# Optimization experiments

Hardware: AMD Instinct MI355X
Metric: run time of the kernel (lower is better)

Reference implementation:

```python
import jax, jax.numpy as jnp
import numpy as np

N = 3072          # num nodes
H = 256           # hidden_features
B = 4             # num_heads
HD = H // B       # per-head dim
PRIOR_MU = 1.0
PRIOR_SIGMA = 1.0
LN_EPS = 1e-5


def setup_inputs() -> dict:
    key = jax.random.key(0)
    ks = jax.random.split(key, 12)
    s = 0.02  # weight init scale
    return {
        "h": jax.random.normal(ks[0], (N, H), jnp.float32),
        "gamma": jnp.ones((H,), jnp.float32),
        "beta": jnp.zeros((H,), jnp.float32),
        "W_k": jax.random.normal(ks[1], (H, H), jnp.float32) * s,
        "b_k": jnp.zeros((H,), jnp.float32),
        "W_mu": jax.random.normal(ks[2], (H, H), jnp.float32) * s,
        "b_mu": jnp.zeros((H,), jnp.float32),
        "W_ls": jax.random.normal(ks[3], (H, H), jnp.float32) * s,
        "b_ls": jnp.zeros((H,), jnp.float32),
        "W_v": jax.random.normal(ks[4], (H * B, H), jnp.float32) * s,
        "b_v": jnp.zeros((H,), jnp.float32),
        "diffusion": jax.random.uniform(ks[5], (N, N, 1), jnp.float32),
        "eps": jax.random.normal(ks[6], (N, N, B), jnp.float32),
    }


def reference(h, gamma, beta, W_k, b_k, W_mu, b_mu, W_ls, b_ls, W_v, b_v, diffusion, eps):
    h0 = h
    # LayerNorm
    mean = jnp.mean(h, axis=-1, keepdims=True)
    var = jnp.var(h, axis=-1, keepdims=True)
    hn = (h - mean) * jax.lax.rsqrt(var + LN_EPS) * gamma + beta
    # Q/K-style projections, split into heads: [N, HD, B]
    k = (hn @ W_k + b_k).reshape(N, HD, B)
    mu = (hn @ W_mu + b_mu).reshape(N, HD, B)
    ls = (hn @ W_ls + b_ls).reshape(N, HD, B)
    scale = HD ** -0.5
    mu = jnp.einsum('xyb,zyb->xzb', k, mu) * scale       # [N, N, B]
    ls = jnp.einsum('xyb,zyb->xzb', k, ls) * scale       # [N, N, B]
    sigma = jax.nn.softplus(ls)
    # KL(LogNormal(mu, sigma) || LogNormal(log(prior_mu), prior_sigma))
    mu_p = jnp.log(jnp.asarray(PRIOR_MU, h.dtype))
    sig_p = jnp.asarray(PRIOR_SIGMA, h.dtype)
    kl = (jnp.log(sig_p / sigma)
          + (sigma ** 2 + (mu - mu_p) ** 2) / (2.0 * sig_p ** 2)
          - 0.5)
    kl = (kl * jnp.sign(diffusion)).sum(-1).mean()
    # reparameterized LogNormal sample, masked by diffusion matrix
    a = jnp.exp(mu + sigma * eps) * diffusion            # [N, N, B]
    # L1 normalize over source-node axis (dim=-2), torch F.normalize semantics
    denom = jnp.clip(jnp.sum(jnp.abs(a), axis=-2, keepdims=True), 1e-12)
    a = a / denom
    # diffusion-weighted aggregation: [N, B, H] -> [N, B*H]
    out = jnp.einsum('xyb,yz->xbz', a, hn).reshape(N, B * H)
    out = out @ W_v + b_v                                 # fc_v (dropout = eval mode)
    out = jax.nn.elu(out) + h0
    return out, kl
```

## Files before the change

### kernel.cpp

```cpp
#include <hip/hip_runtime.h>
#include <hip/hip_bf16.h>


#define NN 3072
#define HH 256
#define NB 4
#define HD 64
constexpr int KMLSZ = 192 * 2 * 64 * 8;

typedef __attribute__((ext_vector_type(8))) short bf16x8;
typedef __attribute__((ext_vector_type(4))) float f32x4;

static __device__ inline short f2bf(float f) {
    __hip_bfloat16 h = __float2bfloat16(f);
    return __builtin_bit_cast(short, h);
}

__global__ void k0_prep(const float* __restrict__ Wk, const float* __restrict__ Wmu,
                        const float* __restrict__ Wls, const float* __restrict__ bk,
                        const float* __restrict__ bmu, const float* __restrict__ bls,
                        const float* __restrict__ Wv, short* __restrict__ WTcat,
                        float* __restrict__ biascat, short* __restrict__ WvT,
                        float* __restrict__ denom) {
    __shared__ float t[64][65];
    int bx = blockIdx.x;
    if (bx < 48) {
        int mat = bx >> 4;
        int by = (bx >> 2) & 3, bc = bx & 3;
        int y0 = by * 64, c0 = bc * 64;
        const float* W = (mat == 0) ? Wk : (mat == 1 ? Wmu : Wls);
        float scale = (mat == 0) ? 0.125f : 1.f;
        int r = threadIdx.x >> 4, c4 = (threadIdx.x & 15) * 4;
#pragma unroll
        for (int i = 0; i < 4; i++) {
            int yl = r + i * 16;
            float4 v = *(const float4*)(W + (y0 + yl) * 256 + c0 + c4);
            t[yl][c4] = v.x; t[yl][c4 + 1] = v.y; t[yl][c4 + 2] = v.z; t[yl][c4 + 3] = v.w;
        }
        __syncthreads();
#pragma unroll
        for (int i = 0; i < 4; i++) {
            int cl = r + i * 16;
            int corig = c0 + cl;
            int cp = mat * 256 + (corig & 3) * 64 + (corig >> 2);
            short4 v = make_short4(f2bf(t[c4][cl] * scale), f2bf(t[c4 + 1][cl] * scale),
                                   f2bf(t[c4 + 2][cl] * scale), f2bf(t[c4 + 3][cl] * scale));
            *(short4*)(WTcat + cp * 256 + y0 + c4) = v;
        }
        return;
    }
    if (bx < 112) {
        int b = bx - 48;
        int bk2 = b >> 2, bn = b & 3;
        int k0 = bk2 * 64, n0 = bn * 64;
        int r = threadIdx.x >> 4, c4 = (threadIdx.x & 15) * 4;
#pragma unroll
        for (int i = 0; i < 4; i++) {
            int kk = r + i * 16;
            float4 v = *(const float4*)(Wv + (k0 + kk) * 256 + n0 + c4);
            t[kk][c4] = v.x; t[kk][c4 + 1] = v.y; t[kk][c4 + 2] = v.z; t[kk][c4 + 3] = v.w;
        }
        __syncthreads();
#pragma unroll
        for (int i = 0; i < 4; i++) {
            int nn = r + i * 16;
            short4 v = make_short4(f2bf(t[c4][nn]), f2bf(t[c4 + 1][nn]),
                                   f2bf(t[c4 + 2][nn]), f2bf(t[c4 + 3][nn]));
            *(short4*)(WvT + (n0 + nn) * 1024 + k0 + c4) = v;
        }
        return;
    }
    if (bx == 112) {
        int cc = threadIdx.x;
        int corig = (cc & 63) * 4 + (cc >> 6);
        biascat[cc] = bk[corig] * 0.125f;
        biascat[256 + cc] = bmu[corig];
        biascat[512 + cc] = bls[corig];
        return;
    }
    int i = (bx - 113) * 256 + threadIdx.x;
    if (i < 13312) denom[i] = 0.f;
}

__global__ void k1_ln(const float* __restrict__ h, const float* __restrict__ gamma,
                      const float* __restrict__ beta, short* __restrict__ hn) {
    int row = blockIdx.x, tid = threadIdx.x;
    float v = h[row * 256 + tid];
    float s = v, s2 = v * v;
    for (int off = 32; off; off >>= 1) {
        s += __shfl_xor(s, off);
        s2 += __shfl_xor(s2, off);
    }
    __shared__ float red[8];
    int w = tid >> 6, lane = tid & 63;
    if (!lane) { red[w] = s; red[4 + w] = s2; }
    __syncthreads();
    s = red[0] + red[1] + red[2] + red[3];
    s2 = red[4] + red[5] + red[6] + red[7];
    float mean = s * (1.f / 256.f);
    float var = s2 * (1.f / 256.f) - mean * mean;
    float rs = rsqrtf(var + 1e-5f);
    hn[row * 256 + tid] = f2bf((v - mean) * rs * gamma[tid] + beta[tid]);
}

__global__ void k1b_tr(const short* __restrict__ hn, short* __restrict__ hnT) {
    __shared__ short t[64][68];
    int bn = blockIdx.x >> 2, bh = blockIdx.x & 3;
    int n0 = bn * 64, h0 = bh * 64;
    int r = threadIdx.x >> 4, c4 = (threadIdx.x & 15) * 4;
#pragma unroll
    for (int i = 0; i < 4; i++) {
        int nn = r + i * 16;
        *(short4*)&t[nn][c4] = *(const short4*)(hn + (n0 + nn) * 256 + h0 + c4);
    }
    __syncthreads();
#pragma unroll
    for (int i = 0; i < 4; i++) {
        int hh = r + i * 16;
        short4 v = make_short4(t[c4][hh], t[c4 + 1][hh], t[c4 + 2][hh], t[c4 + 3][hh]);
        *(short4*)(hnT + (h0 + hh) * NN + n0 + c4) = v;
    }
}

__global__ __launch_bounds__(256) void k2_proj(const short* __restrict__ hn,
                                               const short* __restrict__ WTcat,
                                               const float* __restrict__ biascat,
                                               short* __restrict__ kml) {
    int bx = blockIdx.x;
    int mt = bx / 12, nb = bx % 12;
    int m0 = mt * 64, n0 = nb * 64;
    int tid = threadIdx.x, w = tid >> 6, lane = tid & 63, q = lane >> 4, c = lane & 15;
    int mrow = m0 + w * 16;
    f32x4 acc[4] = {{0, 0, 0, 0}, {0, 0, 0, 0}, {0, 0, 0, 0}, {0, 0, 0, 0}};
    for (int k0 = 0; k0 < 256; k0 += 32) {
        bf16x8 af = *(const bf16x8*)(hn + (mrow + c) * 256 + k0 + q * 8);
#pragma unroll
        for (int nt = 0; nt < 4; nt++) {
            bf16x8 bf = *(const bf16x8*)(WTcat + (n0 + nt * 16 + c) * 256 + k0 + q * 8);
            acc[nt] = __builtin_amdgcn_mfma_f32_16x16x32_bf16(af, bf, acc[nt], 0, 0, 0);
        }
    }
#pragma unroll
    for (int nt = 0; nt < 4; nt++) {
        int cp = n0 + nt * 16 + c;
        float bias = biascat[cp];
        int mat = cp >> 8, b = (cp >> 6) & 3, y = cp & 63;
        short* dst = kml + (size_t)(mat * 4 + b) * KMLSZ;
        int kh2 = y >> 5, lq = (y >> 3) & 3, j = y & 7;
        int zt = mt * 4 + w;
#pragma unroll
        for (int r = 0; r < 4; r++) {
            int ml = 4 * q + r;
            dst[(((zt * 2 + kh2) * 64) + lq * 16 + ml) * 8 + j] = f2bf(acc[nt][r] + bias);
        }
    }
}

__global__ __launch_bounds__(256) void k3a_elem(
    const short* __restrict__ kml, const float* __restrict__ eps,
    const float* __restrict__ diff, short* __restrict__ apk,
    float* __restrict__ denom, float* __restrict__ klsum) {
    __shared__ float klred[4];
    const int tid = threadIdx.x;
    const int w = tid >> 6, lane = tid & 63, q = lane >> 4, c = lane & 15;
    const int swz = (blockIdx.x & 7) * 288 + (blockIdx.x >> 3);
    const int xb = swz % 48;
    const int zc = swz / 48;
    const int xt = xb * 4 + w;
    const int x0 = xt * 16;

    bf16x8 qf[NB][2];
#pragma unroll
    for (int b = 0; b < NB; b++)
#pragma unroll
        for (int kh = 0; kh < 2; kh++)
            qf[b][kh] = *(const bf16x8*)(kml + (size_t)b * KMLSZ +
                                         ((xt * 2 + kh) * 64 + lane) * 8);

    float den_acc[NB] = {0.f, 0.f, 0.f, 0.f};
    float kl_acc = 0.f;
    const size_t xrow = (size_t)(x0 + c) * NN;

    f32x4 e_nxt[4];
    float d_nxt[4];
    {
        const int z16 = zc * 64;
#pragma unroll
        for (int r = 0; r < 4; r++) {
            e_nxt[r] = __builtin_nontemporal_load(
                (const f32x4*)(eps + (xrow + (size_t)(z16 + 4 * q + r)) * 4));
            d_nxt[r] = __builtin_nontemporal_load(diff + xrow + z16 + 4 * q + r);
        }
    }

#pragma unroll
    for (int t = 0; t < 4; t++) {
        const int zt2 = zc * 4 + t;
        f32x4 e4[4];
        float dif[4];
#pragma unroll
        for (int r = 0; r < 4; r++) { e4[r] = e_nxt[r]; dif[r] = d_nxt[r]; }
        if (t < 3) {
            const int z16 = (zt2 + 1) * 16;
#pragma unroll
            for (int r = 0; r < 4; r++) {
                e_nxt[r] = __builtin_nontemporal_load(
                    (const f32x4*)(eps + (xrow + (size_t)(z16 + 4 * q + r)) * 4));
                d_nxt[r] = __builtin_nontemporal_load(diff + xrow + z16 + 4 * q + r);
            }
        }
#pragma unroll
        for (int b = 0; b < NB; b++) {
            const short* mup = kml + (size_t)(NB + b) * KMLSZ;
            const short* lsp = kml + (size_t)(2 * NB + b) * KMLSZ;
            bf16x8 a0 = *(const bf16x8*)(mup + ((zt2 * 2 + 0) * 64 + lane) * 8);
            bf16x8 a1 = *(const bf16x8*)(mup + ((zt2 * 2 + 1) * 64 + lane) * 8);
            bf16x8 l0 = *(const bf16x8*)(lsp + ((zt2 * 2 + 0) * 64 + lane) * 8);
            bf16x8 l1 = *(const bf16x8*)(lsp + ((zt2 * 2 + 1) * 64 + lane) * 8);
            f32x4 smu = {0.f, 0.f, 0.f, 0.f};
            smu = __builtin_amdgcn_mfma_f32_16x16x32_bf16(a0, qf[b][0], smu, 0, 0, 0);
            smu = __builtin_amdgcn_mfma_f32_16x16x32_bf16(a1, qf[b][1], smu, 0, 0, 0);
            f32x4 sls = {0.f, 0.f, 0.f, 0.f};
            sls = __builtin_amdgcn_mfma_f32_16x16x32_bf16(l0, qf[b][0], sls, 0, 0, 0);
            sls = __builtin_amdgcn_mfma_f32_16x16x32_bf16(l1, qf[b][1], sls, 0, 0, 0);
            short pk[4];
#pragma unroll
            for (int r = 0; r < 4; r++) {
                float mu = smu[r];
                float ls = sls[r];
                float e = e4[r][b];
                float d = dif[r];
                float ex = __expf(-fabsf(ls));
                float sg = fmaxf(ls, 0.f) + __logf(1.f + ex);
                float kle = -__logf(sg) + 0.5f * (sg * sg + mu * mu) - 0.5f;
                float sgn = (d > 0.f) ? 1.f : ((d < 0.f) ? -1.f : 0.f);
                kl_acc += sgn * kle;
                float av = __expf(mu + sg * e) * d;
                den_acc[b] += fabsf(av);
                pk[r] = f2bf(av);
            }
            *(short4*)(apk + (((size_t)b * 192 + xt) * 192 + zt2) * 256 + c * 16 + q * 4) =
                make_short4(pk[0], pk[1], pk[2], pk[3]);
        }
    }
#pragma unroll
    for (int b = 0; b < NB; b++) {
        float d = den_acc[b];
        d += __shfl_down(d, 32);
        d += __shfl_down(d, 16);
        if (q == 0) atomicAdd(&denom[(x0 + c) * NB + b], d);
    }
    for (int off = 32; off; off >>= 1) kl_acc += __shfl_xor(kl_acc, off);
    if (lane == 0) klred[w] = kl_acc;
    __syncthreads();
    if (tid == 0) atomicAdd(klsum, klred[0] + klred[1] + klred[2] + klred[3]);
}

__global__ __launch_bounds__(256) void k3b_agg(
    const short* __restrict__ apk, const short* __restrict__ hnT,
    const float* __restrict__ denom, short* __restrict__ aggn) {
    const int tid = threadIdx.x;
    const int w = tid >> 6, lane = tid & 63, q = lane >> 4, c = lane & 15;
    const int q2 = q >> 1, q1 = q & 1;
    const int bid = blockIdx.x;
    const int b = bid & 3;
    const int mb = bid >> 2;
    const int m0 = mb * 32;
    const int n0 = w * 64;

    f32x4 acc[2][4];
#pragma unroll
    for (int i = 0; i < 2; i++)
#pragma unroll
        for (int j = 0; j < 4; j++) acc[i][j] = (f32x4){0.f, 0.f, 0.f, 0.f};

    const short* abase = apk + ((size_t)b * 192 + mb * 2) * 192 * 256 + c * 16 + q1 * 8;
    const short* bbase = hnT + (size_t)(n0 + c) * NN + q * 8;

#define LDA(KS, MT) (*(const bf16x8*)(abase + (size_t)((MT)*192 + (KS)*2 + q2) * 256))
#define LDB(KS, NT) (*(const bf16x8*)(bbase + (size_t)(NT)*16 * NN + (KS)*32))
#define PREF(AF, BF, KS)                                       \
    do {                                                       \
        AF##0 = LDA(KS, 0); AF##1 = LDA(KS, 1);                \
        BF##0 = LDB(KS, 0); BF##1 = LDB(KS, 1);                \
        BF##2 = LDB(KS, 2); BF##3 = LDB(KS, 3);                \
    } while (0)
#define MFMA8(AF, BF)                                                           \
    do {                                                                        \
        acc[0][0] = __builtin_amdgcn_mfma_f32_16x16x32_bf16(AF##0, BF##0, acc[0][0], 0, 0, 0); \
        acc[0][1] = __builtin_amdgcn_mfma_f32_16x16x32_bf16(AF##0, BF##1, acc[0][1], 0, 0, 0); \
        acc[0][2] = __builtin_amdgcn_mfma_f32_16x16x32_bf16(AF##0, BF##2, acc[0][2], 0, 0, 0); \
        acc[0][3] = __builtin_amdgcn_mfma_f32_16x16x32_bf16(AF##0, BF##3, acc[0][3], 0, 0, 0); \
        acc[1][0] = __builtin_amdgcn_mfma_f32_16x16x32_bf16(AF##1, BF##0, acc[1][0], 0, 0, 0); \
        acc[1][1] = __builtin_amdgcn_mfma_f32_16x16x32_bf16(AF##1, BF##1, acc[1][1], 0, 0, 0); \
        acc[1][2] = __builtin_amdgcn_mfma_f32_16x16x32_bf16(AF##1, BF##2, acc[1][2], 0, 0, 0); \
        acc[1][3] = __builtin_amdgcn_mfma_f32_16x16x32_bf16(AF##1, BF##3, acc[1][3], 0, 0, 0); \
    } while (0)

    bf16x8 afA0, afA1, bfA0, bfA1, bfA2, bfA3;
    bf16x8 afB0, afB1, bfB0, bfB1, bfB2, bfB3;
    PREF(afA, bfA, 0);
    PREF(afB, bfB, 1);
    for (int ks = 0; ks < 96; ks += 2) {
        MFMA8(afA, bfA);
        if (ks + 2 < 96) PREF(afA, bfA, ks + 2);
        MFMA8(afB, bfB);
        if (ks + 3 < 96) PREF(afB, bfB, ks + 3);
    }
#undef LDA
#undef LDB
#undef PREF
#undef MFMA8

#pragma unroll
    for (int mt = 0; mt < 2; mt++)
#pragma unroll
        for (int r = 0; r < 4; r++) {
            int x = m0 + mt * 16 + 4 * q + r;
            float rcp = 1.f / fmaxf(denom[x * 4 + b], 1e-12f);
#pragma unroll
            for (int nt = 0; nt < 4; nt++)
                aggn[(size_t)x * 1024 + b * 256 + n0 + nt * 16 + c] =
                    f2bf(acc[mt][nt][r] * rcp);
        }
}

__global__ __launch_bounds__(256) void k4_out(const short* __restrict__ aggn,
                                              const short* __restrict__ WvT,
                                              const float* __restrict__ bv,
                                              const float* __restrict__ h,
                                              const float* __restrict__ klsum,
                                              float* __restrict__ out) {
    int bx = blockIdx.x;
    int mt = bx >> 2, nb = bx & 3;
    int m0 = mt * 64, n0 = nb * 64;
    int tid = threadIdx.x, w = tid >> 6, lane = tid & 63, q = lane >> 4, c = lane & 15;
    int mrow = m0 + w * 16;
    f32x4 acc[4] = {{0, 0, 0, 0}, {0, 0, 0, 0}, {0, 0, 0, 0}, {0, 0, 0, 0}};
    for (int k0 = 0; k0 < 1024; k0 += 32) {
        bf16x8 af = *(const bf16x8*)(aggn + (mrow + c) * 1024 + k0 + q * 8);
#pragma unroll
        for (int nt = 0; nt < 4; nt++) {
            bf16x8 bf = *(const bf16x8*)(WvT + (n0 + nt * 16 + c) * 1024 + k0 + q * 8);
            acc[nt] = __builtin_amdgcn_mfma_f32_16x16x32_bf16(af, bf, acc[nt], 0, 0, 0);
        }
    }
#pragma unroll
    for (int nt = 0; nt < 4; nt++) {
        int col = n0 + nt * 16 + c;
        float bias = bv[col];
#pragma unroll
        for (int r = 0; r < 4; r++) {
            int row = mrow + 4 * q + r;
            float v = acc[nt][r] + bias;
            v = (v > 0.f) ? v : (__expf(v) - 1.f);
            out[row * 256 + col] = v + h[row * 256 + col];
        }
    }
    if (bx == 0 && tid == 0) out[786432] = klsum[0] * (1.0f / 9437184.0f);
}

extern "C" void kernel_launch(void* const* d_in, const int* in_sizes, int n_in,
                              void* d_out, int out_size, void* d_ws, size_t ws_size,
                              hipStream_t stream) {
    const float* h = (const float*)d_in[0];
    const float* gamma = (const float*)d_in[1];
    const float* beta = (const float*)d_in[2];
    const float* Wk = (const float*)d_in[3];
    const float* bk = (const float*)d_in[4];
    const float* Wmu = (const float*)d_in[5];
    const float* bmu = (const float*)d_in[6];
    const float* Wls = (const float*)d_in[7];
    const float* bls = (const float*)d_in[8];
    const float* Wv = (const float*)d_in[9];
    const float* bv = (const float*)d_in[10];
    const float* diff = (const float*)d_in[11];
    const float* eps = (const float*)d_in[12];
    float* out = (float*)d_out;

    char* p = (char*)d_ws;
    short* apk = (short*)p;    p += (size_t)75497472;
    float* denom = (float*)p;  p += 49152;
    float* klsum = (float*)p;  p += 4096;
    short* hn = (short*)p;     p += 1572864;
    short* hnT = (short*)p;    p += 1572864;
    short* kml = (short*)p;    p += 4718592;
    short* WTcat = (short*)p;  p += 393216;
    float* biasc = (float*)p;  p += 4096;
    short* WvT = (short*)p;    p += 524288;
    short* aggn = (short*)p;

    k0_prep<<<165, 256, 0, stream>>>(Wk, Wmu, Wls, bk, bmu, bls, Wv, WTcat, biasc, WvT,
                                     denom);
    k1_ln<<<3072, 256, 0, stream>>>(h, gamma, beta, hn);
    k1b_tr<<<192, 256, 0, stream>>>(hn, hnT);
    k2_proj<<<576, 256, 0, stream>>>(hn, WTcat, biasc, kml);
    k3a_elem<<<48 * 48, 256, 0, stream>>>(kml, eps, diff, apk, denom, klsum);
    k3b_agg<<<384, 256, 0, stream>>>(apk, hnT, denom, aggn);
    k4_out<<<192, 256, 0, stream>>>(aggn, WvT, bv, h, klsum, out);
}
```

Before: 471.4 us.

## Batch MFMA fragment loads, vectorize diffusion loads, split aggregation N, prefetch fc_v

The elementwise kernel now loads the diffusion values for four columns with one vector load instead of four scalar loads. It also gathers the mu and log-sigma fragments for all heads up front and separates the groups with sched barriers, so more memory loads are in flight before the MFMAs run. The aggregation kernel splits the hidden dimension in half, launching twice as many blocks with smaller per-wave tiles and a three-stage register prefetch, to raise occupancy on a grid that was under-filled. The fc_v kernel gains double-buffered register prefetch of its operand fragments, at the cost of more live registers.

```diff
diff --git a/kernel.cpp b/kernel.cpp
--- a/kernel.cpp
+++ b/kernel.cpp
@@ -182,54 +182,73 @@
     const size_t xrow = (size_t)(x0 + c) * NN;
 
     f32x4 e_nxt[4];
-    float d_nxt[4];
+    f32x4 d_nxt;
     {
         const int z16 = zc * 64;
 #pragma unroll
-        for (int r = 0; r < 4; r++) {
+        for (int r = 0; r < 4; r++)
             e_nxt[r] = __builtin_nontemporal_load(
                 (const f32x4*)(eps + (xrow + (size_t)(z16 + 4 * q + r)) * 4));
-            d_nxt[r] = __builtin_nontemporal_load(diff + xrow + z16 + 4 * q + r);
-        }
+        d_nxt = __builtin_nontemporal_load((const f32x4*)(diff + xrow + z16 + 4 * q));
     }
 
 #pragma unroll
     for (int t = 0; t < 4; t++) {
         const int zt2 = zc * 4 + t;
         f32x4 e4[4];
-        float dif[4];
-#pragma unroll
-        for (int r = 0; r < 4; r++) { e4[r] = e_nxt[r]; dif[r] = d_nxt[r]; }
+        f32x4 d4 = d_nxt;
+#pragma unroll
+        for (int r = 0; r < 4; r++) e4[r] = e_nxt[r];
+
+        bf16x8 fr[8];
+#pragma unroll
+        for (int b = 0; b < NB; b++) {
+            const short* mup = kml + (size_t)(NB + b) * KMLSZ;
+            fr[b * 2 + 0] = *(const bf16x8*)(mup + ((zt2 * 2 + 0) * 64 + lane) * 8);
+            fr[b * 2 + 1] = *(const bf16x8*)(mup + ((zt2 * 2 + 1) * 64 + lane) * 8);
+        }
+        __builtin_amdgcn_sched_barrier(0);
+        f32x4 smu[NB];
+#pragma unroll
+        for (int b = 0; b < NB; b++) {
+            f32x4 z4 = {0.f, 0.f, 0.f, 0.f};
+            z4 = __builtin_amdgcn_mfma_f32_16x16x32_bf16(fr[b * 2 + 0], qf[b][0], z4, 0, 0, 0);
+            z4 = __builtin_amdgcn_mfma_f32_16x16x32_bf16(fr[b * 2 + 1], qf[b][1], z4, 0, 0, 0);
+            smu[b] = z4;
+        }
+        bf16x8 fl[8];
+#pragma unroll
+        for (int b = 0; b < NB; b++) {
+            const short* lsp = kml + (size_t)(2 * NB + b) * KMLSZ;
+            fl[b * 2 + 0] = *(const bf16x8*)(lsp + ((zt2 * 2 + 0) * 64 + lane) * 8);
+            fl[b * 2 + 1] = *(const bf16x8*)(lsp + ((zt2 * 2 + 1) * 64 + lane) * 8);
+        }
         if (t < 3) {
             const int z16 = (zt2 + 1) * 16;
 #pragma unroll
-            for (int r = 0; r < 4; r++) {
+            for (int r = 0; r < 4; r++)
                 e_nxt[r] = __builtin_nontemporal_load(
                     (const f32x4*)(eps + (xrow + (size_t)(z16 + 4 * q + r)) * 4));
-                d_nxt[r] = __builtin_nontemporal_load(diff + xrow + z16 + 4 * q + r);
-            }
-        }
+            d_nxt = __builtin_nontemporal_load((const f32x4*)(diff + xrow + z16 + 4 * q));
+        }
+        __builtin_amdgcn_sched_barrier(0);
+        f32x4 sls[NB];
 #pragma unroll
         for (int b = 0; b < NB; b++) {
-            const short* mup = kml + (size_t)(NB + b) * KMLSZ;
-            const short* lsp = kml + (size_t)(2 * NB + b) * KMLSZ;
-            bf16x8 a0 = *(const bf16x8*)(mup + ((zt2 * 2 + 0) * 64 + lane) * 8);
-            bf16x8 a1 = *(const bf16x8*)(mup + ((zt2 * 2 + 1) * 64 + lane) * 8);
-            bf16x8 l0 = *(const bf16x8*)(lsp + ((zt2 * 2 + 0) * 64 + lane) * 8);
-            bf16x8 l1 = *(const bf16x8*)(lsp + ((zt2 * 2 + 1) * 64 + lane) * 8);
-            f32x4 smu = {0.f, 0.f, 0.f, 0.f};
-            smu = __builtin_amdgcn_mfma_f32_16x16x32_bf16(a0, qf[b][0], smu, 0, 0, 0);
-            smu = __builtin_amdgcn_mfma_f32_16x16x32_bf16(a1, qf[b][1], smu, 0, 0, 0);
-            f32x4 sls = {0.f, 0.f, 0.f, 0.f};
-            sls = __builtin_amdgcn_mfma_f32_16x16x32_bf16(l0, qf[b][0], sls, 0, 0, 0);
-            sls = __builtin_amdgcn_mfma_f32_16x16x32_bf16(l1, qf[b][1], sls, 0, 0, 0);
+            f32x4 y4 = {0.f, 0.f, 0.f, 0.f};
+            y4 = __builtin_amdgcn_mfma_f32_16x16x32_bf16(fl[b * 2 + 0], qf[b][0], y4, 0, 0, 0);
+            y4 = __builtin_amdgcn_mfma_f32_16x16x32_bf16(fl[b * 2 + 1], qf[b][1], y4, 0, 0, 0);
+            sls[b] = y4;
+        }
+#pragma unroll
+        for (int b = 0; b < NB; b++) {
             short pk[4];
 #pragma unroll
             for (int r = 0; r < 4; r++) {
-                float mu = smu[r];
-                float ls = sls[r];
+                float mu = smu[b][r];
+                float ls = sls[b][r];
                 float e = e4[r][b];
-                float d = dif[r];
+                float d = d4[r];
                 float ex = __expf(-fabsf(ls));
                 float sg = fmaxf(ls, 0.f) + __logf(1.f + ex);
                 float kle = -__logf(sg) + 0.5f * (sg * sg + mu * mu) - 0.5f;
@@ -263,54 +282,55 @@
     const int w = tid >> 6, lane = tid & 63, q = lane >> 4, c = lane & 15;
     const int q2 = q >> 1, q1 = q & 1;
     const int bid = blockIdx.x;
-    const int b = bid & 3;
-    const int mb = bid >> 2;
+    const int nh = bid / 384;
+    const int r2 = bid % 384;
+    const int b = r2 & 3;
+    const int mb = r2 >> 2;
     const int m0 = mb * 32;
-    const int n0 = w * 64;
-
-    f32x4 acc[2][4];
+    const int n0 = nh * 128 + w * 32;
+
+    f32x4 acc[2][2];
 #pragma unroll
     for (int i = 0; i < 2; i++)
 #pragma unroll
-        for (int j = 0; j < 4; j++) acc[i][j] = (f32x4){0.f, 0.f, 0.f, 0.f};
+        for (int j = 0; j < 2; j++) acc[i][j] = (f32x4){0.f, 0.f, 0.f, 0.f};
 
     const short* abase = apk + ((size_t)b * 192 + mb * 2) * 192 * 256 + c * 16 + q1 * 8;
     const short* bbase = hnT + (size_t)(n0 + c) * NN + q * 8;
 
-#define LDA(KS, MT) (*(const bf16x8*)(abase + (size_t)((MT)*192 + (KS)*2 + q2) * 256))
-#define LDB(KS, NT) (*(const bf16x8*)(bbase + (size_t)(NT)*16 * NN + (KS)*32))
-#define PREF(AF, BF, KS)                                       \
+#define LDA(KS, MT) (*(const bf16x8*)(abase + (size_t)((MT) * 192 + (KS) * 2 + q2) * 256))
+#define LDB(KS, NT) (*(const bf16x8*)(bbase + (size_t)(NT) * 16 * NN + (KS) * 32))
+#define PREF(S, KS)                                            \
     do {                                                       \
-        AF##0 = LDA(KS, 0); AF##1 = LDA(KS, 1);                \
-        BF##0 = LDB(KS, 0); BF##1 = LDB(KS, 1);                \
-        BF##2 = LDB(KS, 2); BF##3 = LDB(KS, 3);                \
+        S##a0 = LDA(KS, 0); S##a1 = LDA(KS, 1);                \
+        S##b0 = LDB(KS, 0); S##b1 = LDB(KS, 1);                \
     } while (0)
-#define MFMA8(AF, BF)                                                           \
-    do {                                                                        \
-        acc[0][0] = __builtin_amdgcn_mfma_f32_16x16x32_bf16(AF##0, BF##0, acc[0][0], 0, 0, 0); \
-        acc[0][1] = __builtin_amdgcn_mfma_f32_16x16x32_bf16(AF##0, BF##1, acc[0][1], 0, 0, 0); \
-        acc[0][2] = __builtin_amdgcn_mfma_f32_16x16x32_bf16(AF##0, BF##2, acc[0][2], 0, 0, 0); \
-        acc[0][3] = __builtin_amdgcn_mfma_f32_16x16x32_bf16(AF##0, BF##3, acc[0][3], 0, 0, 0); \
-        acc[1][0] = __builtin_amdgcn_mfma_f32_16x16x32_bf16(AF##1, BF##0, acc[1][0], 0, 0, 0); \
-        acc[1][1] = __builtin_amdgcn_mfma_f32_16x16x32_bf16(AF##1, BF##1, acc[1][1], 0, 0, 0); \
-        acc[1][2] = __builtin_amdgcn_mfma_f32_16x16x32_bf16(AF##1, BF##2, acc[1][2], 0, 0, 0); \
-        acc[1][3] = __builtin_amdgcn_mfma_f32_16x16x32_bf16(AF##1, BF##3, acc[1][3], 0, 0, 0); \
+#define MFMA4(S)                                                                        \
+    do {                                                                                \
+        acc[0][0] = __builtin_amdgcn_mfma_f32_16x16x32_bf16(S##a0, S##b0, acc[0][0], 0, 0, 0); \
+        acc[0][1] = __builtin_amdgcn_mfma_f32_16x16x32_bf16(S##a0, S##b1, acc[0][1], 0, 0, 0); \
+        acc[1][0] = __builtin_amdgcn_mfma_f32_16x16x32_bf16(S##a1, S##b0, acc[1][0], 0, 0, 0); \
+        acc[1][1] = __builtin_amdgcn_mfma_f32_16x16x32_bf16(S##a1, S##b1, acc[1][1], 0, 0, 0); \
     } while (0)
 
-    bf16x8 afA0, afA1, bfA0, bfA1, bfA2, bfA3;
-    bf16x8 afB0, afB1, bfB0, bfB1, bfB2, bfB3;
-    PREF(afA, bfA, 0);
-    PREF(afB, bfB, 1);
-    for (int ks = 0; ks < 96; ks += 2) {
-        MFMA8(afA, bfA);
-        if (ks + 2 < 96) PREF(afA, bfA, ks + 2);
-        MFMA8(afB, bfB);
-        if (ks + 3 < 96) PREF(afB, bfB, ks + 3);
+    bf16x8 Pa0, Pa1, Pb0, Pb1;
+    bf16x8 Qa0, Qa1, Qb0, Qb1;
+    bf16x8 Ra0, Ra1, Rb0, Rb1;
+    PREF(P, 0);
+    PREF(Q, 1);
+    PREF(R, 2);
+    for (int ks = 0; ks < 96; ks += 3) {
+        MFMA4(P);
+        if (ks + 3 < 96) PREF(P, ks + 3);
+        MFMA4(Q);
+        if (ks + 4 < 96) PREF(Q, ks + 4);
+        MFMA4(R);
+        if (ks + 5 < 96) PREF(R, ks + 5);
     }
 #undef LDA
 #undef LDB
 #undef PREF
-#undef MFMA8
+#undef MFMA4
 
 #pragma unroll
     for (int mt = 0; mt < 2; mt++)
@@ -319,7 +339,7 @@
             int x = m0 + mt * 16 + 4 * q + r;
             float rcp = 1.f / fmaxf(denom[x * 4 + b], 1e-12f);
 #pragma unroll
-            for (int nt = 0; nt < 4; nt++)
+            for (int nt = 0; nt < 2; nt++)
                 aggn[(size_t)x * 1024 + b * 256 + n0 + nt * 16 + c] =
                     f2bf(acc[mt][nt][r] * rcp);
         }
@@ -337,14 +357,40 @@
     int tid = threadIdx.x, w = tid >> 6, lane = tid & 63, q = lane >> 4, c = lane & 15;
     int mrow = m0 + w * 16;
     f32x4 acc[4] = {{0, 0, 0, 0}, {0, 0, 0, 0}, {0, 0, 0, 0}, {0, 0, 0, 0}};
-    for (int k0 = 0; k0 < 1024; k0 += 32) {
-        bf16x8 af = *(const bf16x8*)(aggn + (mrow + c) * 1024 + k0 + q * 8);
-#pragma unroll
-        for (int nt = 0; nt < 4; nt++) {
-            bf16x8 bf = *(const bf16x8*)(WvT + (n0 + nt * 16 + c) * 1024 + k0 + q * 8);
-            acc[nt] = __builtin_amdgcn_mfma_f32_16x16x32_bf16(af, bf, acc[nt], 0, 0, 0);
-        }
-    }
+    const short* abase = aggn + (mrow + c) * 1024 + q * 8;
+    const short* bbase = WvT + (n0 + c) * 1024 + q * 8;
+
+#define LDA4(KS) (*(const bf16x8*)(abase + (KS) * 32))
+#define LDB4(KS, NT) (*(const bf16x8*)(bbase + (NT) * 16 * 1024 + (KS) * 32))
+#define PREF4(S, KS)                                                    \
+    do {                                                                \
+        S##a = LDA4(KS);                                                \
+        S##b0 = LDB4(KS, 0); S##b1 = LDB4(KS, 1);                       \
+        S##b2 = LDB4(KS, 2); S##b3 = LDB4(KS, 3);                       \
+    } while (0)
+#define MFMA4K(S)                                                                      \
+    do {                                                                               \
+        acc[0] = __builtin_amdgcn_mfma_f32_16x16x32_bf16(S##a, S##b0, acc[0], 0, 0, 0); \
+        acc[1] = __builtin_amdgcn_mfma_f32_16x16x32_bf16(S##a, S##b1, acc[1], 0, 0, 0); \
+        acc[2] = __builtin_amdgcn_mfma_f32_16x16x32_bf16(S##a, S##b2, acc[2], 0, 0, 0); \
+        acc[3] = __builtin_amdgcn_mfma_f32_16x16x32_bf16(S##a, S##b3, acc[3], 0, 0, 0); \
+    } while (0)
+
+    bf16x8 Pa, Pb0, Pb1, Pb2, Pb3;
+    bf16x8 Qa, Qb0, Qb1, Qb2, Qb3;
+    PREF4(P, 0);
+    PREF4(Q, 1);
+    for (int ks = 0; ks < 32; ks += 2) {
+        MFMA4K(P);
+        if (ks + 2 < 32) PREF4(P, ks + 2);
+        MFMA4K(Q);
+        if (ks + 3 < 32) PREF4(Q, ks + 3);
+    }
+#undef LDA4
+#undef LDB4
+#undef PREF4
+#undef MFMA4K
+
 #pragma unroll
     for (int nt = 0; nt < 4; nt++) {
         int col = n0 + nt * 16 + c;
@@ -396,6 +442,6 @@
     k1b_tr<<<192, 256, 0, stream>>>(hn, hnT);
     k2_proj<<<576, 256, 0, stream>>>(hn, WTcat, biasc, kml);
     k3a_elem<<<48 * 48, 256, 0, stream>>>(kml, eps, diff, apk, denom, klsum);
-    k3b_agg<<<384, 256, 0, stream>>>(apk, hnT, denom, aggn);
+    k3b_agg<<<768, 256, 0, stream>>>(apk, hnT, denom, aggn);
     k4_out<<<192, 256, 0, stream>>>(aggn, WvT, bv, h, klsum, out);
 }
```

Measured after the change: 471.4 us. About the same (+0.0%).
